# Kernel optimization log

Measured on AMD Instinct MI355X. Metric: run time of the kernel, lower is better.

Reference implementation:

```python
import jax, jax.numpy as jnp
import numpy as np
from jax import lax

V, D = 50000, 300          # vocab, word_embed_dim
C, K, H = 256, 3, 256      # conv out_channels, kernel_size, hidden_size
HLU, AH, NC = 512, 256, 2  # hidden_layer_units, attn_hidden, num_classes
B, QL, AL = 64, 40, 60     # batch, question len, answer len
EPS_COS, EPS_BN = 1e-6, 1e-5


def setup_inputs() -> dict:
    key = jax.random.key(0)
    ks = jax.random.split(key, 16)
    r = lambda k, shp: (0.02 * jax.random.normal(k, shp)).astype(jnp.float32)
    return {
        "question": jax.random.randint(ks[0], (B, QL), 0, V, dtype=jnp.int32),
        "answer": jax.random.randint(ks[1], (B, AL), 0, V, dtype=jnp.int32),
        "ext_feats": jnp.zeros((B, 2), jnp.float32),
        "embedding": r(ks[2], (V, D)),
        # sm_cnn (shared for question and answer)
        "sm_convW": r(ks[3], (K, D, C)), "sm_convb": jnp.zeros((C,), jnp.float32),
        "sm_fcW": r(ks[4], (C, H)), "sm_fcb": jnp.zeros((H,), jnp.float32),
        # context_cnn
        "ctx_convW": r(ks[5], (K, D, C)), "ctx_convb": jnp.zeros((C,), jnp.float32),
        "ctx_fcW": r(ks[6], (C, H)), "ctx_fcb": jnp.zeros((H,), jnp.float32),
        # cnn_attn MLP + cnn_prob
        "attnW": r(ks[7], (H + D, AH)), "attnb": jnp.zeros((AH,), jnp.float32),
        "probW": r(ks[8], (AH, 1)),
        # final_layers: Linear(3H, HLU) + BatchNorm1d
        "W1": r(ks[9], (3 * H, HLU)), "b1": jnp.zeros((HLU,), jnp.float32),
        "gamma": jnp.ones((HLU,), jnp.float32), "beta": jnp.zeros((HLU,), jnp.float32),
        # softmax head
        "W2": r(ks[10], (HLU, NC)), "b2": jnp.zeros((NC,), jnp.float32),
    }


def _simple_cnn(x, convW, convb, fcW, fcb):
    # x: [N, L, D]; full-width Kim-CNN == conv1d over time with D input channels
    y = lax.conv_general_dilated(x, convW, (1,), 'VALID',
                                 dimension_numbers=('NWC', 'WIO', 'NWC'))
    y = jax.nn.relu(y + convb)        # [N, L-K+1, C]
    y = jnp.max(y, axis=1)            # max-pool over time -> [N, C]
    return y @ fcW + fcb              # [N, H]


def reference(question, answer, ext_feats, embedding,
              sm_convW, sm_convb, sm_fcW, sm_fcb,
              ctx_convW, ctx_convb, ctx_fcW, ctx_fcb,
              attnW, attnb, probW, W1, b1, gamma, beta, W2, b2):
    sent1 = embedding[question]                    # [B, QL, D]
    sent2 = embedding[answer]                      # [B, AL, D]

    feature1 = _simple_cnn(sent1, sm_convW, sm_convb, sm_fcW, sm_fcb)   # [B, H]
    feature2 = _simple_cnn(sent2, sm_convW, sm_convb, sm_fcW, sm_fcb)   # [B, H]

    # ---- attn_context (gating_source == 'embed') ----
    nq = jnp.linalg.norm(sent1, axis=-1)           # [B, QL]
    na = jnp.linalg.norm(sent2, axis=-1)           # [B, AL]
    dots = jnp.einsum('bqd,bad->bqa', sent1, sent2)
    cos = dots / jnp.maximum(nq[:, :, None] * na[:, None, :], EPS_COS)  # [B, QL, AL]
    attn_answer = sent2[:, None, :, :] * cos[..., None]                 # [B, QL, AL, D]
    attn_answer = attn_answer.reshape(B * QL, AL, D)

    feat = _simple_cnn(attn_answer, ctx_convW, ctx_convb, ctx_fcW, ctx_fcb)  # [B*QL, H]
    qa_comb = jnp.concatenate([feat, sent1.reshape(-1, D)], axis=1)          # [B*QL, H+D]
    score = (jnp.tanh(qa_comb @ attnW + attnb) @ probW).reshape(B, QL)
    cnn_prob = jax.nn.softmax(score, axis=1)                                 # [B, QL]
    feature3 = jnp.sum(feat.reshape(B, QL, H) * cnn_prob[..., None], axis=1)  # [B, H]

    # ---- final layers ----
    feat_comb = jnp.concatenate([feature1, feature2, feature3], axis=1)  # [B, 3H]
    h = feat_comb @ W1 + b1
    mu = jnp.mean(h, axis=0)
    var = jnp.mean((h - mu) ** 2, axis=0)          # biased, BN training mode
    h = (h - mu) / jnp.sqrt(var + EPS_BN) * gamma + beta
    feat_out = jnp.tanh(h)                          # dropout = identity (p=0)

    preds = jax.nn.log_softmax(feat_out @ W2 + b2, axis=1)
    return preds, feat_out
```

## Files before the change

kernel.cpp:

```cpp
#include <hip/hip_runtime.h>
#include <math.h>

#define Bn 64
#define QLn 40
#define ALn 60
#define Dn 300
#define KS 640
#define NQ 1024
#define NA 1536

typedef __attribute__((ext_vector_type(8))) short bf16x8;
typedef __attribute__((ext_vector_type(4))) float f32x4;

__device__ __forceinline__ float bf2f(unsigned short s) {
  return __uint_as_float(((unsigned)s) << 16);
}
__device__ __forceinline__ short f2bf(float f) {
  unsigned u = __float_as_uint(f);
  unsigned r = (u + 0x7FFFu + ((u >> 16) & 1u)) >> 16;
  return (short)r;
}

__global__ __launch_bounds__(256) void k_prep(
    const int* __restrict__ qIdx, const int* __restrict__ aIdx,
    const float* __restrict__ emb,
    const float* __restrict__ smW, const float* __restrict__ ctxW,
    const float* __restrict__ attnW, const float* __restrict__ ctxfcW,
    const float* __restrict__ ctxfcb, const float* __restrict__ attnb,
    short* __restrict__ Ae1, short* __restrict__ Ae2,
    float* __restrict__ nq, float* __restrict__ na,
    short* __restrict__ BTall, float* __restrict__ Wcat, float* __restrict__ bvec) {
  __shared__ float lds[4160];
  int bid = blockIdx.x, tid = threadIdx.x;
  int w = tid >> 6, lane = tid & 63;
  if (bid < 1600) {
    int row = bid * 4 + w;
    const int* idxp; short* Ae; float* nrm; int r;
    if (row < 2560) { idxp = qIdx; Ae = Ae1; nrm = nq; r = row; }
    else { idxp = aIdx; Ae = Ae2; nrm = na; r = row - 2560; }
    int tok = idxp[r];
    const float4* src = (const float4*)(emb + (size_t)tok * Dn);
    short* d = Ae + (size_t)r * KS;
    float ssq = 0.f;
    for (int i = lane; i < 80; i += 64) {
      float4 v = (i < 75) ? src[i] : make_float4(0.f, 0.f, 0.f, 0.f);
      ssq += v.x * v.x + v.y * v.y + v.z * v.z + v.w * v.w;
      short4 h4, l4v;
      h4.x = f2bf(v.x); l4v.x = f2bf(v.x - bf2f((unsigned short)h4.x));
      h4.y = f2bf(v.y); l4v.y = f2bf(v.y - bf2f((unsigned short)h4.y));
      h4.z = f2bf(v.z); l4v.z = f2bf(v.z - bf2f((unsigned short)h4.z));
      h4.w = f2bf(v.w); l4v.w = f2bf(v.w - bf2f((unsigned short)h4.w));
      *(short4*)&d[i * 4] = h4;
      *(short4*)&d[320 + i * 4] = l4v;
    }
    #pragma unroll
    for (int o = 32; o; o >>= 1) ssq += __shfl_down(ssq, o, 64);
    if (lane == 0) nrm[r] = sqrtf(ssq);
  } else if (bid < 1800) {
    int tb = bid - 1600;
    int kt = tb % 5, nt = tb / 5;
    int n0 = nt * 64;
    const float* src; int cb;
    if (n0 < 768)       { src = smW + (n0 >> 8) * 76800; cb = n0 & 255; }
    else if (n0 < 1024) { src = attnW + 65536;           cb = n0 - 768; }
    else if (n0 < 1792) { int m = n0 - 1024; src = smW + (m >> 8) * 76800; cb = m & 255; }
    else                { int m = n0 - 1792; src = ctxW + (m >> 8) * 76800; cb = m & 255; }
    float* tile = lds;
    int nn = tid & 63;
    #pragma unroll
    for (int it = 0; it < 16; ++it) {
      int kl = it * 4 + w;
      int k = kt * 64 + kl;
      tile[kl * 65 + nn] = (k < 300) ? src[(size_t)k * 256 + cb + nn] : 0.f;
    }
    __syncthreads();
    #pragma unroll
    for (int it = 0; it < 16; ++it) {
      int nloc = it * 4 + w;
      int kl = tid & 63;
      float v = tile[kl * 65 + nloc];
      int n = n0 + nloc, k = kt * 64 + kl;
      short hi = f2bf(v), lo = f2bf(v - bf2f((unsigned short)hi));
      BTall[(size_t)n * KS + k] = hi;
      BTall[(size_t)n * KS + 320 + k] = lo;
    }
  } else {
    int k = bid - 1800;
    float* rowv = lds;
    int j = tid;
    rowv[j] = (k < 256) ? ctxfcW[(size_t)k * 256 + j] : ctxfcb[j];
    __syncthreads();
    float a0 = 0.f, a1 = 0.f, a2 = 0.f, a3 = 0.f;
    for (int m = 0; m < 256; m += 4) {
      a0 += rowv[m]     * attnW[(size_t)m * 256 + j];
      a1 += rowv[m + 1] * attnW[(size_t)(m + 1) * 256 + j];
      a2 += rowv[m + 2] * attnW[(size_t)(m + 2) * 256 + j];
      a3 += rowv[m + 3] * attnW[(size_t)(m + 3) * 256 + j];
    }
    float acc = (a0 + a1) + (a2 + a3);
    if (k < 256) {
      Wcat[(size_t)k * 512 + j] = rowv[j];
      Wcat[(size_t)k * 512 + 256 + j] = acc;
    } else {
      bvec[j] = ctxfcb[j];
      bvec[256 + j] = acc + attnb[j];
    }
  }
}

__device__ __forceinline__ void gl2lds16(const short* g, short* l) {
  __builtin_amdgcn_global_load_lds(
      (const __attribute__((address_space(1))) unsigned int*)g,
      (__attribute__((address_space(3))) unsigned int*)l, 16, 0, 0);
}

__global__ __launch_bounds__(256) void k_mega(
    const short* __restrict__ Ae1, const short* __restrict__ Ae2,
    const short* __restrict__ BTall, float* __restrict__ ZQ, float* __restrict__ ZA,
    const float* __restrict__ nq, const float* __restrict__ na,
    float* __restrict__ cosb) {
  __shared__ __align__(16) short As[128 * 32];
  __shared__ __align__(16) short Bs[128 * 32];
  int tid = threadIdx.x;
  int wid = tid >> 6, lane = tid & 63;
  int l15 = lane & 15, l4 = lane >> 4;
  int bid = blockIdx.x;
  int lin = (bid & 7) * 73 + (bid >> 3);

  if (lin < 520) {
    const short *A, *BT; float* C; int bx, by, ldc;
    if (lin < 160) {
      int chunk = lin >> 4, ww = lin & 15;
      by = ww >> 1; bx = chunk * 2 + (ww & 1);
      A = Ae1; BT = BTall; C = ZQ; ldc = NQ;
    } else {
      int l2 = lin - 160;
      int chunk = l2 / 24, ww = l2 % 24;
      by = ww >> 1; bx = chunk * 2 + (ww & 1);
      A = Ae2; BT = BTall + (size_t)1024 * KS; C = ZA; ldc = NA;
    }
    int rowBase = bx * 128, colBase = by * 128;
    int mw = wid * 32;

    f32x4 acc[2][8];
    #pragma unroll
    for (int i = 0; i < 2; ++i)
      #pragma unroll
      for (int j = 0; j < 8; ++j) acc[i][j] = (f32x4){0.f, 0.f, 0.f, 0.f};

    int rowA0 = mw + l15, rowA1 = mw + 16 + l15;
    int sA0 = (l4 ^ ((rowA0 >> 1) & 3)) << 3;
    int sA1 = (l4 ^ ((rowA1 >> 1) & 3)) << 3;

    #pragma unroll 1
    for (int g = 0; g < 3; ++g) {
      int aoff = (g == 1) ? 320 : 0;
      int boff = (g == 2) ? 320 : 0;
      #pragma unroll 1
      for (int ks = 0; ks < 10; ++ks) {
        int ka0 = aoff + ks * 32, kb0 = boff + ks * 32;
        #pragma unroll
        for (int j = 0; j < 2; ++j) {
          int idx = tid + j * 256;
          int r = idx >> 2, s = idx & 3;
          int sl = s ^ ((r >> 1) & 3);
          int chunkStart = j * 256 + wid * 64;
          gl2lds16(A + (size_t)(rowBase + r) * KS + ka0 + (sl << 3), &As[chunkStart * 8]);
          gl2lds16(BT + (size_t)(colBase + r) * KS + kb0 + (sl << 3), &Bs[chunkStart * 8]);
        }
        __syncthreads();
        bf16x8 a0 = *reinterpret_cast<const bf16x8*>(&As[rowA0 * 32 + sA0]);
        bf16x8 a1 = *reinterpret_cast<const bf16x8*>(&As[rowA1 * 32 + sA1]);
        #pragma unroll
        for (int nj = 0; nj < 8; ++nj) {
          int rb = nj * 16 + l15;
          bf16x8 bf = *reinterpret_cast<const bf16x8*>(&Bs[rb * 32 + ((l4 ^ ((rb >> 1) & 3)) << 3)]);
          acc[0][nj] = __builtin_amdgcn_mfma_f32_16x16x32_bf16(a0, bf, acc[0][nj], 0, 0, 0);
          acc[1][nj] = __builtin_amdgcn_mfma_f32_16x16x32_bf16(a1, bf, acc[1][nj], 0, 0, 0);
        }
        __syncthreads();
      }
    }
    #pragma unroll
    for (int mi = 0; mi < 2; ++mi) {
      int row0 = rowBase + mw + mi * 16 + l4 * 4;
      #pragma unroll
      for (int nj = 0; nj < 8; ++nj) {
        int col = colBase + nj * 16 + l15;
        #pragma unroll
        for (int r = 0; r < 4; ++r)
          C[(size_t)(row0 + r) * ldc + col] = acc[mi][nj][r];
      }
    }
  } else {
    int b = lin - 520;
    int rowBase = b * 40, colBase = b * 60;
    f32x4 cacc[4];
    #pragma unroll
    for (int nj = 0; nj < 4; ++nj) cacc[nj] = (f32x4){0.f, 0.f, 0.f, 0.f};
    int rowA = (wid << 4) + l15;
    int sA = (l4 ^ ((rowA >> 1) & 3)) << 3;

    #pragma unroll 1
    for (int g = 0; g < 3; ++g) {
      int aoff = (g == 1) ? 320 : 0;
      int boff = (g == 2) ? 320 : 0;
      #pragma unroll 1
      for (int ks = 0; ks < 10; ++ks) {
        int ka0 = aoff + ks * 32, kb0 = boff + ks * 32;
        int r = tid >> 2, s = tid & 3;
        int sl = s ^ ((r >> 1) & 3);
        int chunkStart = wid * 64;
        int gr = rowBase + r; if (gr > 2559) gr = 2559;
        int gc = colBase + r; if (gc > 3839) gc = 3839;
        gl2lds16(Ae1 + (size_t)gr * KS + ka0 + (sl << 3), &As[chunkStart * 8]);
        gl2lds16(Ae2 + (size_t)gc * KS + kb0 + (sl << 3), &Bs[chunkStart * 8]);
        __syncthreads();
        bf16x8 a0 = *reinterpret_cast<const bf16x8*>(&As[rowA * 32 + sA]);
        #pragma unroll
        for (int nj = 0; nj < 4; ++nj) {
          int rb = (nj << 4) + l15;
          bf16x8 bf = *reinterpret_cast<const bf16x8*>(&Bs[rb * 32 + ((l4 ^ ((rb >> 1) & 3)) << 3)]);
          cacc[nj] = __builtin_amdgcn_mfma_f32_16x16x32_bf16(a0, bf, cacc[nj], 0, 0, 0);
        }
        __syncthreads();
      }
    }
    int q0 = (wid << 4) + l4 * 4;
    #pragma unroll
    for (int nj = 0; nj < 4; ++nj) {
      int a = (nj << 4) + l15;
      if (a >= ALn) continue;
      float nav = na[colBase + a];
      #pragma unroll
      for (int r = 0; r < 4; ++r) {
        int qq = q0 + r;
        if (qq < QLn) {
          float den = fmaxf(nq[rowBase + qq] * nav, 1e-6f);
          cosb[(size_t)(rowBase + qq) * ALn + a] = cacc[nj][r] / den;
        }
      }
    }
  }
}

__global__ void k_poolctx(const float* __restrict__ ZQ, const float* __restrict__ ZA,
                          const float* __restrict__ convb, const float* __restrict__ cosb,
                          const float* __restrict__ ctxb,
                          float* __restrict__ pooled_part, float* __restrict__ pctx_part) {
  __shared__ float cl[10][ALn];
  int bid = blockIdx.x, tid = threadIdx.x;
  if (bid < 256) {
    int blk = bid & 127, half = bid >> 7;
    int c = tid;
    const float* base; int P, ld;
    if (blk < Bn) { base = ZQ + (size_t)blk * QLn * NQ; P = QLn - 2; ld = NQ; }
    else          { base = ZA + (size_t)(blk - Bn) * ALn * NA; P = ALn - 2; ld = NA; }
    int t0 = half * (P >> 1), t1 = (half ? P : (P >> 1));
    float bias = convb[c];
    float m = 0.f;
    #pragma unroll 4
    for (int t = t0; t < t1; ++t) {
      float v = bias + base[t * ld + c] + base[(t + 1) * ld + 256 + c]
                     + base[(t + 2) * ld + 512 + c];
      m = fmaxf(m, v);
    }
    pooled_part[((size_t)half * 128 + blk) * 256 + c] = m;
  } else {
    int bid2 = bid - 256;
    int b = bid2 & 63, sub = bid2 >> 6;
    int qg = sub >> 1, th = sub & 1;
    int c = tid;
    for (int i = tid; i < 10 * ALn; i += 256) {
      int qq = i / ALn, tt = i % ALn;
      cl[qq][tt] = cosb[((size_t)b * QLn + qg * 10 + qq) * ALn + tt];
    }
    __syncthreads();
    const float* base = ZA + (size_t)b * ALn * NA + 768;
    float bias = ctxb[c];
    float m[10];
    #pragma unroll
    for (int qq = 0; qq < 10; ++qq) m[qq] = 0.f;
    int t0 = th * 29;
    #pragma unroll 2
    for (int t = t0; t < t0 + 29; ++t) {
      float v0 = base[t * NA + c];
      float v1 = base[(t + 1) * NA + 256 + c];
      float v2 = base[(t + 2) * NA + 512 + c];
      #pragma unroll
      for (int qq = 0; qq < 10; ++qq) {
        float v = bias + cl[qq][t] * v0 + cl[qq][t + 1] * v1 + cl[qq][t + 2] * v2;
        m[qq] = fmaxf(m[qq], v);
      }
    }
    #pragma unroll
    for (int qq = 0; qq < 10; ++qq)
      pctx_part[((size_t)th * 2560 + (size_t)b * QLn + qg * 10 + qq) * 256 + c] = m[qq];
  }
}

__global__ __launch_bounds__(256) void k_fcattn(
    const float* __restrict__ pooled_part, const float* __restrict__ smfcW,
    const float* __restrict__ smfcb,
    const float* __restrict__ pctx_part, const float* __restrict__ Wcat,
    const float* __restrict__ bvec, const float* __restrict__ ZQ,
    const float* __restrict__ probW,
    float* __restrict__ feat_comb, float* __restrict__ feat, float* __restrict__ score) {
  __shared__ float lds[10304];
  int bid = blockIdx.x, j = threadIdx.x;
  if (bid < 32) {
    float* xin = lds;
    float* wt  = lds + 1024;
    int r0 = bid * 4;
    #pragma unroll
    for (int rr = 0; rr < 4; ++rr)
      xin[j * 4 + rr] = fmaxf(pooled_part[(size_t)(r0 + rr) * 256 + j],
                              pooled_part[(size_t)(128 + r0 + rr) * 256 + j]);
    float acc[4];
    #pragma unroll
    for (int rr = 0; rr < 4; ++rr) acc[rr] = smfcb[j];
    for (int ph = 0; ph < 8; ++ph) {
      const float4* src = (const float4*)(smfcW + (size_t)ph * 32 * 256);
      float4* dst = (float4*)wt;
      #pragma unroll
      for (int i = 0; i < 8; ++i) dst[i * 256 + j] = src[i * 256 + j];
      __syncthreads();
      #pragma unroll
      for (int kk = 0; kk < 32; ++kk) {
        float4 x = *reinterpret_cast<const float4*>(&xin[(ph * 32 + kk) * 4]);
        float wv = wt[kk * 256 + j];
        acc[0] += x.x * wv; acc[1] += x.y * wv; acc[2] += x.z * wv; acc[3] += x.w * wv;
      }
      __syncthreads();
    }
    #pragma unroll
    for (int rr = 0; rr < 4; ++rr) {
      int row = r0 + rr;
      feat_comb[(size_t)(row & 63) * 768 + ((row >> 6) * 256) + j] = acc[rr];
    }
  } else {
    float* xin  = lds;
    float* wt   = lds + 2048;
    float* sred = lds + 10240;
    int r0 = (bid - 32) * 8;
    #pragma unroll
    for (int rr = 0; rr < 8; ++rr)
      xin[j * 8 + rr] = fmaxf(pctx_part[(size_t)(r0 + rr) * 256 + j],
                              pctx_part[(size_t)(2560 + r0 + rr) * 256 + j]);
    float hf[8], hh[8];
    float bf0 = bvec[j], bh0 = bvec[256 + j];
    #pragma unroll
    for (int rr = 0; rr < 8; ++rr) {
      hf[rr] = bf0;
      hh[rr] = bh0 + ZQ[(size_t)(r0 + rr) * NQ + 768 + j];
    }
    for (int ph = 0; ph < 16; ++ph) {
      const float4* src = (const float4*)(Wcat + (size_t)ph * 16 * 512);
      float4* dst = (float4*)wt;
      #pragma unroll
      for (int i = 0; i < 8; ++i) dst[i * 256 + j] = src[i * 256 + j];
      __syncthreads();
      #pragma unroll
      for (int kk = 0; kk < 16; ++kk) {
        int k = ph * 16 + kk;
        float4 x0 = *reinterpret_cast<const float4*>(&xin[k * 8]);
        float4 x1 = *reinterpret_cast<const float4*>(&xin[k * 8 + 4]);
        float w0 = wt[kk * 512 + j], w1 = wt[kk * 512 + 256 + j];
        hf[0] += x0.x * w0; hf[1] += x0.y * w0; hf[2] += x0.z * w0; hf[3] += x0.w * w0;
        hf[4] += x1.x * w0; hf[5] += x1.y * w0; hf[6] += x1.z * w0; hf[7] += x1.w * w0;
        hh[0] += x0.x * w1; hh[1] += x0.y * w1; hh[2] += x0.z * w1; hh[3] += x0.w * w1;
        hh[4] += x1.x * w1; hh[5] += x1.y * w1; hh[6] += x1.z * w1; hh[7] += x1.w * w1;
      }
      __syncthreads();
    }
    #pragma unroll
    for (int rr = 0; rr < 8; ++rr)
      feat[(size_t)(r0 + rr) * 256 + j] = hf[rr];
    float pw = probW[j];
    int lane = j & 63, wv = j >> 6;
    #pragma unroll
    for (int rr = 0; rr < 8; ++rr) {
      float s = tanhf(hh[rr]) * pw;
      #pragma unroll
      for (int off = 32; off; off >>= 1) s += __shfl_down(s, off, 64);
      if (lane == 0) sred[rr * 4 + wv] = s;
    }
    __syncthreads();
    if (j < 8) score[r0 + j] = sred[j * 4] + sred[j * 4 + 1] + sred[j * 4 + 2] + sred[j * 4 + 3];
  }
}

__global__ void k_attnpool(const float* __restrict__ score, const float* __restrict__ feat,
                           float* __restrict__ feat_comb) {
  int b = blockIdx.x;
  int tid = threadIdx.x;
  __shared__ float p[QLn];
  __shared__ float inv;
  if (tid < 64) {
    float sc = (tid < QLn) ? score[b * QLn + tid] : -1e30f;
    float mx = sc;
    #pragma unroll
    for (int off = 32; off; off >>= 1) mx = fmaxf(mx, __shfl_xor(mx, off, 64));
    float e = (tid < QLn) ? expf(sc - mx) : 0.f;
    if (tid < QLn) p[tid] = e;
    float den = e;
    #pragma unroll
    for (int off = 32; off; off >>= 1) den += __shfl_xor(den, off, 64);
    if (tid == 0) inv = 1.f / den;
  }
  __syncthreads();
  float acc = 0.f;
  for (int qq = 0; qq < QLn; ++qq)
    acc += p[qq] * feat[((size_t)b * QLn + qq) * 256 + tid];
  feat_comb[(size_t)b * 768 + 512 + tid] = acc * inv;
}

__global__ __launch_bounds__(256) void k_w1bn(
    const float* __restrict__ feat_comb, const float* __restrict__ W1,
    const float* __restrict__ b1, const float* __restrict__ gamma,
    const float* __restrict__ beta, float* __restrict__ feat_out) {
  int j0 = blockIdx.x * 8;
  int tid = threadIdx.x;
  __shared__ float wl[768][12];
  __shared__ float hb[64][8];
  for (int it = 0; it < 24; ++it) {
    int idx = tid + it * 256;
    int k = idx >> 3, jj = idx & 7;
    wl[k][jj] = W1[(size_t)k * 512 + j0 + jj];
  }
  __syncthreads();
  int n = tid >> 2, p = tid & 3;
  float acc[8] = {0.f, 0.f, 0.f, 0.f, 0.f, 0.f, 0.f, 0.f};
  const float* frow = feat_comb + (size_t)n * 768 + p;
  for (int i = 0; i < 192; ++i) {
    float v = frow[i * 4];
    int k = p + i * 4;
    float4 w0 = *reinterpret_cast<const float4*>(&wl[k][0]);
    float4 w1v = *reinterpret_cast<const float4*>(&wl[k][4]);
    acc[0] += v * w0.x; acc[1] += v * w0.y; acc[2] += v * w0.z; acc[3] += v * w0.w;
    acc[4] += v * w1v.x; acc[5] += v * w1v.y; acc[6] += v * w1v.z; acc[7] += v * w1v.w;
  }
  #pragma unroll
  for (int jj = 0; jj < 8; ++jj) {
    acc[jj] += __shfl_xor(acc[jj], 1, 64);
    acc[jj] += __shfl_xor(acc[jj], 2, 64);
  }
  if (p == 0) {
    #pragma unroll
    for (int jj = 0; jj < 8; ++jj) hb[n][jj] = acc[jj] + b1[j0 + jj];
  }
  __syncthreads();
  if (tid < 64) {
    #pragma unroll
    for (int jj = 0; jj < 8; ++jj) {
      float v = hb[tid][jj];
      float s = v;
      #pragma unroll
      for (int off = 32; off; off >>= 1) s += __shfl_xor(s, off, 64);
      float mu = s * (1.f / 64.f);
      float d = v - mu;
      float q2 = d * d;
      #pragma unroll
      for (int off = 32; off; off >>= 1) q2 += __shfl_xor(q2, off, 64);
      float var = q2 * (1.f / 64.f);
      feat_out[(size_t)tid * 512 + j0 + jj] =
          tanhf(d * rsqrtf(var + 1e-5f) * gamma[j0 + jj] + beta[j0 + jj]);
    }
  }
}

__global__ void k_head(const float* __restrict__ feat_out, const float* __restrict__ W2,
                       const float* __restrict__ b2, float* __restrict__ preds) {
  int n = blockIdx.x;
  int tid = threadIdx.x;
  float a0 = 0.f, a1 = 0.f;
  for (int j = tid; j < 512; j += 64) {
    float f = feat_out[(size_t)n * 512 + j];
    a0 += f * W2[j * 2 + 0];
    a1 += f * W2[j * 2 + 1];
  }
  #pragma unroll
  for (int off = 32; off; off >>= 1) {
    a0 += __shfl_down(a0, off, 64);
    a1 += __shfl_down(a1, off, 64);
  }
  if (tid == 0) {
    float l0 = a0 + b2[0], l1 = a1 + b2[1];
    float mx = fmaxf(l0, l1);
    float lse = mx + logf(expf(l0 - mx) + expf(l1 - mx));
    preds[n * 2 + 0] = l0 - lse;
    preds[n * 2 + 1] = l1 - lse;
  }
}

extern "C" void kernel_launch(void* const* d_in, const int* in_sizes, int n_in,
                              void* d_out, int out_size, void* d_ws, size_t ws_size,
                              hipStream_t stream) {
  (void)in_sizes; (void)n_in; (void)out_size; (void)ws_size;
  const int*   question  = (const int*)d_in[0];
  const int*   answer    = (const int*)d_in[1];
  const float* embedding = (const float*)d_in[3];
  const float* sm_convW  = (const float*)d_in[4];
  const float* sm_convb  = (const float*)d_in[5];
  const float* sm_fcW    = (const float*)d_in[6];
  const float* sm_fcb    = (const float*)d_in[7];
  const float* ctx_convW = (const float*)d_in[8];
  const float* ctx_convb = (const float*)d_in[9];
  const float* ctx_fcW   = (const float*)d_in[10];
  const float* ctx_fcb   = (const float*)d_in[11];
  const float* attnW     = (const float*)d_in[12];
  const float* attnb     = (const float*)d_in[13];
  const float* probW     = (const float*)d_in[14];
  const float* W1        = (const float*)d_in[15];
  const float* b1        = (const float*)d_in[16];
  const float* gamma     = (const float*)d_in[17];
  const float* beta      = (const float*)d_in[18];
  const float* W2        = (const float*)d_in[19];
  const float* b2        = (const float*)d_in[20];

  float* out = (float*)d_out;
  char* base = (char*)d_ws;
  size_t off = 0;
  auto alloc = [&](size_t bytes) { char* p = base + off; off += (bytes + 255) & ~(size_t)255; return p; };

  short* Ae1   = (short*)alloc(2560ull * KS * 2);
  short* Ae2   = (short*)alloc(3840ull * KS * 2);
  short* BTall = (short*)alloc(2560ull * KS * 2);
  float* ZQ    = (float*)alloc(2560ull * NQ * 4);
  float* ZA    = (float*)alloc(3840ull * NA * 4);
  float* nq    = (float*)alloc(2560 * 4);
  float* na    = (float*)alloc(3840 * 4);
  float* cosb  = (float*)alloc(2560ull * ALn * 4);
  float* Wcat  = (float*)alloc(256ull * 512 * 4);
  float* bvec  = (float*)alloc(512 * 4);
  float* pctx_part = (float*)alloc(2ull * 2560 * 256 * 4);
  float* feat      = (float*)alloc(2560ull * 256 * 4);
  float* feat_comb = (float*)alloc(64ull * 768 * 4);
  float* score     = (float*)alloc(2560 * 4);
  float* pooled_part = (float*)BTall;

  k_prep<<<2057, 256, 0, stream>>>(question, answer, embedding, sm_convW, ctx_convW,
                                   attnW, ctx_fcW, ctx_fcb, attnb,
                                   Ae1, Ae2, nq, na, BTall, Wcat, bvec);
  k_mega<<<584, 256, 0, stream>>>(Ae1, Ae2, BTall, ZQ, ZA, nq, na, cosb);
  k_poolctx<<<768, 256, 0, stream>>>(ZQ, ZA, sm_convb, cosb, ctx_convb,
                                     pooled_part, pctx_part);
  k_fcattn<<<352, 256, 0, stream>>>(pooled_part, sm_fcW, sm_fcb,
                                    pctx_part, Wcat, bvec, ZQ, probW,
                                    feat_comb, feat, score);
  k_attnpool<<<Bn, 256, 0, stream>>>(score, feat, feat_comb);
  k_w1bn<<<64, 256, 0, stream>>>(feat_comb, W1, b1, gamma, beta, out + 128);
  k_head<<<Bn, 64, 0, stream>>>(out + 128, W2, b2, out);
}
```

Before: 113.6 us.

## Fuse pooling, attention softmax and head into fewer kernels with bf16 intermediates

The GEMM outputs ZQ/ZA are now stored as bf16 instead of fp32, which halves the intermediate traffic. The max-pool and context-pool kernel is folded into k_fcattn. The attention softmax pooling is replaced by atomic accumulation of an unnormalized numerator and denominator, and the W2 log-softmax head is merged into k_w1bn using a last-block counter. This cuts the launch count from seven to four and removes several global round-trips. In exchange it adds bf16 rounding of the conv outputs, drops the max subtraction in the softmax exp (overflow risk), and relies on float atomics, so results are nondeterministic. Pool work in the 32 sm blocks is now serial over the full length, which may lengthen that tail.

```diff
diff --git a/kernel.cpp b/kernel.cpp
--- a/kernel.cpp
+++ b/kernel.cpp
@@ -29,7 +29,9 @@
     const float* __restrict__ ctxfcb, const float* __restrict__ attnb,
     short* __restrict__ Ae1, short* __restrict__ Ae2,
     float* __restrict__ nq, float* __restrict__ na,
-    short* __restrict__ BTall, float* __restrict__ Wcat, float* __restrict__ bvec) {
+    short* __restrict__ BTall, float* __restrict__ Wcat, float* __restrict__ bvec,
+    float* __restrict__ numb, float* __restrict__ denb,
+    float* __restrict__ logits, int* __restrict__ done) {
   __shared__ float lds[4160];
   int bid = blockIdx.x, tid = threadIdx.x;
   int w = tid >> 6, lane = tid & 63;
@@ -84,7 +86,7 @@
       BTall[(size_t)n * KS + k] = hi;
       BTall[(size_t)n * KS + 320 + k] = lo;
     }
-  } else {
+  } else if (bid < 2057) {
     int k = bid - 1800;
     float* rowv = lds;
     int j = tid;
@@ -105,6 +107,11 @@
       bvec[j] = ctxfcb[j];
       bvec[256 + j] = acc + attnb[j];
     }
+  } else {
+    for (int i = tid; i < Bn * 256; i += 256) numb[i] = 0.f;
+    if (tid < Bn) denb[tid] = 0.f;
+    if (tid < 2 * Bn) logits[tid] = 0.f;
+    if (tid == 0) *done = 0;
   }
 }
 
@@ -116,7 +123,7 @@
 
 __global__ __launch_bounds__(256) void k_mega(
     const short* __restrict__ Ae1, const short* __restrict__ Ae2,
-    const short* __restrict__ BTall, float* __restrict__ ZQ, float* __restrict__ ZA,
+    const short* __restrict__ BTall, short* __restrict__ ZQb, short* __restrict__ ZAb,
     const float* __restrict__ nq, const float* __restrict__ na,
     float* __restrict__ cosb) {
   __shared__ __align__(16) short As[128 * 32];
@@ -128,16 +135,16 @@
   int lin = (bid & 7) * 73 + (bid >> 3);
 
   if (lin < 520) {
-    const short *A, *BT; float* C; int bx, by, ldc;
+    const short *A, *BT; short* C; int bx, by, ldc;
     if (lin < 160) {
       int chunk = lin >> 4, ww = lin & 15;
       by = ww >> 1; bx = chunk * 2 + (ww & 1);
-      A = Ae1; BT = BTall; C = ZQ; ldc = NQ;
+      A = Ae1; BT = BTall; C = ZQb; ldc = NQ;
     } else {
       int l2 = lin - 160;
       int chunk = l2 / 24, ww = l2 % 24;
       by = ww >> 1; bx = chunk * 2 + (ww & 1);
-      A = Ae2; BT = BTall + (size_t)1024 * KS; C = ZA; ldc = NA;
+      A = Ae2; BT = BTall + (size_t)1024 * KS; C = ZAb; ldc = NA;
     }
     int rowBase = bx * 128, colBase = by * 128;
     int mw = wid * 32;
@@ -189,7 +196,7 @@
         int col = colBase + nj * 16 + l15;
         #pragma unroll
         for (int r = 0; r < 4; ++r)
-          C[(size_t)(row0 + r) * ldc + col] = acc[mi][nj][r];
+          C[(size_t)(row0 + r) * ldc + col] = f2bf(acc[mi][nj][r]);
       }
     }
   } else {
@@ -244,78 +251,35 @@
   }
 }
 
-__global__ void k_poolctx(const float* __restrict__ ZQ, const float* __restrict__ ZA,
-                          const float* __restrict__ convb, const float* __restrict__ cosb,
-                          const float* __restrict__ ctxb,
-                          float* __restrict__ pooled_part, float* __restrict__ pctx_part) {
-  __shared__ float cl[10][ALn];
-  int bid = blockIdx.x, tid = threadIdx.x;
-  if (bid < 256) {
-    int blk = bid & 127, half = bid >> 7;
-    int c = tid;
-    const float* base; int P, ld;
-    if (blk < Bn) { base = ZQ + (size_t)blk * QLn * NQ; P = QLn - 2; ld = NQ; }
-    else          { base = ZA + (size_t)(blk - Bn) * ALn * NA; P = ALn - 2; ld = NA; }
-    int t0 = half * (P >> 1), t1 = (half ? P : (P >> 1));
-    float bias = convb[c];
-    float m = 0.f;
-    #pragma unroll 4
-    for (int t = t0; t < t1; ++t) {
-      float v = bias + base[t * ld + c] + base[(t + 1) * ld + 256 + c]
-                     + base[(t + 2) * ld + 512 + c];
-      m = fmaxf(m, v);
-    }
-    pooled_part[((size_t)half * 128 + blk) * 256 + c] = m;
-  } else {
-    int bid2 = bid - 256;
-    int b = bid2 & 63, sub = bid2 >> 6;
-    int qg = sub >> 1, th = sub & 1;
-    int c = tid;
-    for (int i = tid; i < 10 * ALn; i += 256) {
-      int qq = i / ALn, tt = i % ALn;
-      cl[qq][tt] = cosb[((size_t)b * QLn + qg * 10 + qq) * ALn + tt];
-    }
-    __syncthreads();
-    const float* base = ZA + (size_t)b * ALn * NA + 768;
-    float bias = ctxb[c];
-    float m[10];
-    #pragma unroll
-    for (int qq = 0; qq < 10; ++qq) m[qq] = 0.f;
-    int t0 = th * 29;
-    #pragma unroll 2
-    for (int t = t0; t < t0 + 29; ++t) {
-      float v0 = base[t * NA + c];
-      float v1 = base[(t + 1) * NA + 256 + c];
-      float v2 = base[(t + 2) * NA + 512 + c];
-      #pragma unroll
-      for (int qq = 0; qq < 10; ++qq) {
-        float v = bias + cl[qq][t] * v0 + cl[qq][t + 1] * v1 + cl[qq][t + 2] * v2;
-        m[qq] = fmaxf(m[qq], v);
-      }
-    }
-    #pragma unroll
-    for (int qq = 0; qq < 10; ++qq)
-      pctx_part[((size_t)th * 2560 + (size_t)b * QLn + qg * 10 + qq) * 256 + c] = m[qq];
-  }
-}
-
 __global__ __launch_bounds__(256) void k_fcattn(
-    const float* __restrict__ pooled_part, const float* __restrict__ smfcW,
-    const float* __restrict__ smfcb,
-    const float* __restrict__ pctx_part, const float* __restrict__ Wcat,
-    const float* __restrict__ bvec, const float* __restrict__ ZQ,
-    const float* __restrict__ probW,
-    float* __restrict__ feat_comb, float* __restrict__ feat, float* __restrict__ score) {
-  __shared__ float lds[10304];
+    const short* __restrict__ ZQb, const short* __restrict__ ZAb,
+    const float* __restrict__ convb, const float* __restrict__ smfcW,
+    const float* __restrict__ smfcb, const float* __restrict__ cosb,
+    const float* __restrict__ ctxb, const float* __restrict__ Wcat,
+    const float* __restrict__ bvec, const float* __restrict__ probW,
+    float* __restrict__ feat_comb, float* __restrict__ numb, float* __restrict__ denb) {
+  __shared__ float lds[10816];
   int bid = blockIdx.x, j = threadIdx.x;
   if (bid < 32) {
     float* xin = lds;
     float* wt  = lds + 1024;
     int r0 = bid * 4;
-    #pragma unroll
-    for (int rr = 0; rr < 4; ++rr)
-      xin[j * 4 + rr] = fmaxf(pooled_part[(size_t)(r0 + rr) * 256 + j],
-                              pooled_part[(size_t)(128 + r0 + rr) * 256 + j]);
+    float bias0 = convb[j];
+    #pragma unroll
+    for (int rr = 0; rr < 4; ++rr) {
+      int s = r0 + rr;
+      const short* zb; int L, ld;
+      if (s < Bn) { zb = ZQb + (size_t)s * QLn * NQ; L = QLn; ld = NQ; }
+      else        { zb = ZAb + (size_t)(s - Bn) * ALn * NA; L = ALn; ld = NA; }
+      float m = 0.f;
+      for (int t = 0; t <= L - 3; ++t) {
+        float v = bias0 + bf2f((unsigned short)zb[t * ld + j])
+                        + bf2f((unsigned short)zb[(t + 1) * ld + 256 + j])
+                        + bf2f((unsigned short)zb[(t + 2) * ld + 512 + j]);
+        m = fmaxf(m, v);
+      }
+      xin[j * 4 + rr] = m;
+    }
     float acc[4];
     #pragma unroll
     for (int rr = 0; rr < 4; ++rr) acc[rr] = smfcb[j];
@@ -336,23 +300,43 @@
     #pragma unroll
     for (int rr = 0; rr < 4; ++rr) {
       int row = r0 + rr;
-      feat_comb[(size_t)(row & 63) * 768 + ((row >> 6) * 256) + j] = acc[rr];
+      feat_comb[(size_t)(row & 63) * 512 + ((row >> 6) * 256) + j] = acc[rr];
     }
   } else {
     float* xin  = lds;
     float* wt   = lds + 2048;
     float* sred = lds + 10240;
-    int r0 = (bid - 32) * 8;
-    #pragma unroll
-    for (int rr = 0; rr < 8; ++rr)
-      xin[j * 8 + rr] = fmaxf(pctx_part[(size_t)(r0 + rr) * 256 + j],
-                              pctx_part[(size_t)(2560 + r0 + rr) * 256 + j]);
+    float* cl   = lds + 10304;
+    int g = bid - 32;
+    int b = g / 5, q0 = (g % 5) * 8;
+    int rq = b * QLn + q0;
+    for (int i = j; i < 8 * ALn; i += 256)
+      cl[(i / ALn) * ALn + (i % ALn)] = cosb[(size_t)(rq + i / ALn) * ALn + (i % ALn)];
+    __syncthreads();
+    const short* zb = ZAb + (size_t)b * ALn * NA + 768;
+    float biasc = ctxb[j];
+    float m[8];
+    #pragma unroll
+    for (int rr = 0; rr < 8; ++rr) m[rr] = 0.f;
+    for (int t = 0; t <= ALn - 3; ++t) {
+      float v0 = bf2f((unsigned short)zb[t * NA + j]);
+      float v1 = bf2f((unsigned short)zb[(t + 1) * NA + 256 + j]);
+      float v2 = bf2f((unsigned short)zb[(t + 2) * NA + 512 + j]);
+      #pragma unroll
+      for (int rr = 0; rr < 8; ++rr) {
+        float v = biasc + cl[rr * ALn + t] * v0 + cl[rr * ALn + t + 1] * v1
+                        + cl[rr * ALn + t + 2] * v2;
+        m[rr] = fmaxf(m[rr], v);
+      }
+    }
+    #pragma unroll
+    for (int rr = 0; rr < 8; ++rr) xin[j * 8 + rr] = m[rr];
     float hf[8], hh[8];
     float bf0 = bvec[j], bh0 = bvec[256 + j];
     #pragma unroll
     for (int rr = 0; rr < 8; ++rr) {
       hf[rr] = bf0;
-      hh[rr] = bh0 + ZQ[(size_t)(r0 + rr) * NQ + 768 + j];
+      hh[rr] = bh0 + bf2f((unsigned short)ZQb[(size_t)(rq + rr) * NQ + 768 + j]);
     }
     for (int ph = 0; ph < 16; ++ph) {
       const float4* src = (const float4*)(Wcat + (size_t)ph * 16 * 512);
@@ -373,9 +357,6 @@
       }
       __syncthreads();
     }
-    #pragma unroll
-    for (int rr = 0; rr < 8; ++rr)
-      feat[(size_t)(r0 + rr) * 256 + j] = hf[rr];
     float pw = probW[j];
     int lane = j & 63, wv = j >> 6;
     #pragma unroll
@@ -386,43 +367,31 @@
       if (lane == 0) sred[rr * 4 + wv] = s;
     }
     __syncthreads();
-    if (j < 8) score[r0 + j] = sred[j * 4] + sred[j * 4 + 1] + sred[j * 4 + 2] + sred[j * 4 + 3];
-  }
-}
-
-__global__ void k_attnpool(const float* __restrict__ score, const float* __restrict__ feat,
-                           float* __restrict__ feat_comb) {
-  int b = blockIdx.x;
-  int tid = threadIdx.x;
-  __shared__ float p[QLn];
-  __shared__ float inv;
-  if (tid < 64) {
-    float sc = (tid < QLn) ? score[b * QLn + tid] : -1e30f;
-    float mx = sc;
-    #pragma unroll
-    for (int off = 32; off; off >>= 1) mx = fmaxf(mx, __shfl_xor(mx, off, 64));
-    float e = (tid < QLn) ? expf(sc - mx) : 0.f;
-    if (tid < QLn) p[tid] = e;
-    float den = e;
-    #pragma unroll
-    for (int off = 32; off; off >>= 1) den += __shfl_xor(den, off, 64);
-    if (tid == 0) inv = 1.f / den;
-  }
-  __syncthreads();
-  float acc = 0.f;
-  for (int qq = 0; qq < QLn; ++qq)
-    acc += p[qq] * feat[((size_t)b * QLn + qq) * 256 + tid];
-  feat_comb[(size_t)b * 768 + 512 + tid] = acc * inv;
+    float e[8], esum = 0.f, acc3 = 0.f;
+    #pragma unroll
+    for (int rr = 0; rr < 8; ++rr) {
+      float s = sred[rr * 4] + sred[rr * 4 + 1] + sred[rr * 4 + 2] + sred[rr * 4 + 3];
+      e[rr] = __expf(s);
+      esum += e[rr];
+      acc3 += e[rr] * hf[rr];
+    }
+    atomicAdd(&numb[(size_t)b * 256 + j], acc3);
+    if (j == 0) atomicAdd(&denb[b], esum);
+  }
 }
 
 __global__ __launch_bounds__(256) void k_w1bn(
-    const float* __restrict__ feat_comb, const float* __restrict__ W1,
+    const float* __restrict__ feat_comb, const float* __restrict__ numb,
+    const float* __restrict__ denb, const float* __restrict__ W1,
     const float* __restrict__ b1, const float* __restrict__ gamma,
-    const float* __restrict__ beta, float* __restrict__ feat_out) {
+    const float* __restrict__ beta, const float* __restrict__ W2,
+    const float* __restrict__ b2, float* __restrict__ feat_out,
+    float* __restrict__ preds, float* __restrict__ logits, int* __restrict__ done) {
   int j0 = blockIdx.x * 8;
   int tid = threadIdx.x;
   __shared__ float wl[768][12];
   __shared__ float hb[64][8];
+  __shared__ int lastflag;
   for (int it = 0; it < 24; ++it) {
     int idx = tid + it * 256;
     int k = idx >> 3, jj = idx & 7;
@@ -430,27 +399,41 @@
   }
   __syncthreads();
   int n = tid >> 2, p = tid & 3;
-  float acc[8] = {0.f, 0.f, 0.f, 0.f, 0.f, 0.f, 0.f, 0.f};
-  const float* frow = feat_comb + (size_t)n * 768 + p;
-  for (int i = 0; i < 192; ++i) {
+  float acc1[8] = {0.f, 0.f, 0.f, 0.f, 0.f, 0.f, 0.f, 0.f};
+  float acc2[8] = {0.f, 0.f, 0.f, 0.f, 0.f, 0.f, 0.f, 0.f};
+  const float* frow = feat_comb + (size_t)n * 512 + p;
+  for (int i = 0; i < 128; ++i) {
     float v = frow[i * 4];
     int k = p + i * 4;
     float4 w0 = *reinterpret_cast<const float4*>(&wl[k][0]);
     float4 w1v = *reinterpret_cast<const float4*>(&wl[k][4]);
-    acc[0] += v * w0.x; acc[1] += v * w0.y; acc[2] += v * w0.z; acc[3] += v * w0.w;
-    acc[4] += v * w1v.x; acc[5] += v * w1v.y; acc[6] += v * w1v.z; acc[7] += v * w1v.w;
+    acc1[0] += v * w0.x; acc1[1] += v * w0.y; acc1[2] += v * w0.z; acc1[3] += v * w0.w;
+    acc1[4] += v * w1v.x; acc1[5] += v * w1v.y; acc1[6] += v * w1v.z; acc1[7] += v * w1v.w;
+  }
+  const float* nrow = numb + (size_t)n * 256 + p;
+  for (int i = 0; i < 64; ++i) {
+    float v = nrow[i * 4];
+    int k = 512 + p + i * 4;
+    float4 w0 = *reinterpret_cast<const float4*>(&wl[k][0]);
+    float4 w1v = *reinterpret_cast<const float4*>(&wl[k][4]);
+    acc2[0] += v * w0.x; acc2[1] += v * w0.y; acc2[2] += v * w0.z; acc2[3] += v * w0.w;
+    acc2[4] += v * w1v.x; acc2[5] += v * w1v.y; acc2[6] += v * w1v.z; acc2[7] += v * w1v.w;
   }
   #pragma unroll
   for (int jj = 0; jj < 8; ++jj) {
-    acc[jj] += __shfl_xor(acc[jj], 1, 64);
-    acc[jj] += __shfl_xor(acc[jj], 2, 64);
+    acc1[jj] += __shfl_xor(acc1[jj], 1, 64);
+    acc1[jj] += __shfl_xor(acc1[jj], 2, 64);
+    acc2[jj] += __shfl_xor(acc2[jj], 1, 64);
+    acc2[jj] += __shfl_xor(acc2[jj], 2, 64);
   }
   if (p == 0) {
-    #pragma unroll
-    for (int jj = 0; jj < 8; ++jj) hb[n][jj] = acc[jj] + b1[j0 + jj];
+    float rden = 1.f / denb[n];
+    #pragma unroll
+    for (int jj = 0; jj < 8; ++jj) hb[n][jj] = acc1[jj] + rden * acc2[jj] + b1[j0 + jj];
   }
   __syncthreads();
   if (tid < 64) {
+    float l0p = 0.f, l1p = 0.f;
     #pragma unroll
     for (int jj = 0; jj < 8; ++jj) {
       float v = hb[tid][jj];
@@ -463,33 +446,26 @@
       #pragma unroll
       for (int off = 32; off; off >>= 1) q2 += __shfl_xor(q2, off, 64);
       float var = q2 * (1.f / 64.f);
-      feat_out[(size_t)tid * 512 + j0 + jj] =
-          tanhf(d * rsqrtf(var + 1e-5f) * gamma[j0 + jj] + beta[j0 + jj]);
-    }
-  }
-}
-
-__global__ void k_head(const float* __restrict__ feat_out, const float* __restrict__ W2,
-                       const float* __restrict__ b2, float* __restrict__ preds) {
-  int n = blockIdx.x;
-  int tid = threadIdx.x;
-  float a0 = 0.f, a1 = 0.f;
-  for (int j = tid; j < 512; j += 64) {
-    float f = feat_out[(size_t)n * 512 + j];
-    a0 += f * W2[j * 2 + 0];
-    a1 += f * W2[j * 2 + 1];
-  }
-  #pragma unroll
-  for (int off = 32; off; off >>= 1) {
-    a0 += __shfl_down(a0, off, 64);
-    a1 += __shfl_down(a1, off, 64);
-  }
-  if (tid == 0) {
-    float l0 = a0 + b2[0], l1 = a1 + b2[1];
+      float fo = tanhf(d * rsqrtf(var + 1e-5f) * gamma[j0 + jj] + beta[j0 + jj]);
+      feat_out[(size_t)tid * 512 + j0 + jj] = fo;
+      l0p += fo * W2[(j0 + jj) * 2 + 0];
+      l1p += fo * W2[(j0 + jj) * 2 + 1];
+    }
+    atomicAdd(&logits[tid * 2 + 0], l0p);
+    atomicAdd(&logits[tid * 2 + 1], l1p);
+  }
+  __threadfence();
+  __syncthreads();
+  if (tid == 0) lastflag = (atomicAdd(done, 1) == gridDim.x - 1) ? 1 : 0;
+  __syncthreads();
+  if (lastflag && tid < 64) {
+    __threadfence();
+    float l0 = atomicAdd(&logits[tid * 2 + 0], 0.f) + b2[0];
+    float l1 = atomicAdd(&logits[tid * 2 + 1], 0.f) + b2[1];
     float mx = fmaxf(l0, l1);
-    float lse = mx + logf(expf(l0 - mx) + expf(l1 - mx));
-    preds[n * 2 + 0] = l0 - lse;
-    preds[n * 2 + 1] = l1 - lse;
+    float lse = mx + logf(__expf(l0 - mx) + __expf(l1 - mx));
+    preds[tid * 2 + 0] = l0 - lse;
+    preds[tid * 2 + 1] = l1 - lse;
   }
 }
 
@@ -526,29 +502,27 @@
   short* Ae1   = (short*)alloc(2560ull * KS * 2);
   short* Ae2   = (short*)alloc(3840ull * KS * 2);
   short* BTall = (short*)alloc(2560ull * KS * 2);
-  float* ZQ    = (float*)alloc(2560ull * NQ * 4);
-  float* ZA    = (float*)alloc(3840ull * NA * 4);
+  short* ZQb   = (short*)alloc(2560ull * NQ * 2);
+  short* ZAb   = (short*)alloc(3840ull * NA * 2);
   float* nq    = (float*)alloc(2560 * 4);
   float* na    = (float*)alloc(3840 * 4);
   float* cosb  = (float*)alloc(2560ull * ALn * 4);
   float* Wcat  = (float*)alloc(256ull * 512 * 4);
   float* bvec  = (float*)alloc(512 * 4);
-  float* pctx_part = (float*)alloc(2ull * 2560 * 256 * 4);
-  float* feat      = (float*)alloc(2560ull * 256 * 4);
-  float* feat_comb = (float*)alloc(64ull * 768 * 4);
-  float* score     = (float*)alloc(2560 * 4);
-  float* pooled_part = (float*)BTall;
-
-  k_prep<<<2057, 256, 0, stream>>>(question, answer, embedding, sm_convW, ctx_convW,
+  float* feat_comb = (float*)alloc(64ull * 512 * 4);
+  float* numb   = (float*)alloc(64ull * 256 * 4);
+  float* denb   = (float*)alloc(64 * 4);
+  float* logits = (float*)alloc(128 * 4);
+  int*   done   = (int*)alloc(256);
+
+  k_prep<<<2058, 256, 0, stream>>>(question, answer, embedding, sm_convW, ctx_convW,
                                    attnW, ctx_fcW, ctx_fcb, attnb,
-                                   Ae1, Ae2, nq, na, BTall, Wcat, bvec);
-  k_mega<<<584, 256, 0, stream>>>(Ae1, Ae2, BTall, ZQ, ZA, nq, na, cosb);
-  k_poolctx<<<768, 256, 0, stream>>>(ZQ, ZA, sm_convb, cosb, ctx_convb,
-                                     pooled_part, pctx_part);
-  k_fcattn<<<352, 256, 0, stream>>>(pooled_part, sm_fcW, sm_fcb,
-                                    pctx_part, Wcat, bvec, ZQ, probW,
-                                    feat_comb, feat, score);
-  k_attnpool<<<Bn, 256, 0, stream>>>(score, feat, feat_comb);
-  k_w1bn<<<64, 256, 0, stream>>>(feat_comb, W1, b1, gamma, beta, out + 128);
-  k_head<<<Bn, 64, 0, stream>>>(out + 128, W2, b2, out);
-}
+                                   Ae1, Ae2, nq, na, BTall, Wcat, bvec,
+                                   numb, denb, logits, done);
+  k_mega<<<584, 256, 0, stream>>>(Ae1, Ae2, BTall, ZQb, ZAb, nq, na, cosb);
+  k_fcattn<<<352, 256, 0, stream>>>(ZQb, ZAb, sm_convb, sm_fcW, sm_fcb, cosb,
+                                    ctx_convb, Wcat, bvec, probW,
+                                    feat_comb, numb, denb);
+  k_w1bn<<<64, 256, 0, stream>>>(feat_comb, numb, denb, W1, b1, gamma, beta,
+                                 W2, b2, out + 128, out, logits, done);
+}
```

New measurement: 121.7 us. +7.1%, slower.
